# Kernel tuning notes

Measured on AMD Instinct MI355X. Metric: run time of the kernel, lower is better.

The kernel has to match this reference:

```python
import jax, jax.numpy as jnp
import numpy as np

N_SEND = 12288   # 12 * 32^2
N_REC = 49152    # 12 * 64^2
E = 196608       # 4 * N_REC (knn with k=4)
D = 256
EIN, EOUT = 4, 256
LIN_IN, LIN_OUT = 512, 256
B = 2


def setup_inputs() -> dict:
    key = jax.random.key(0)
    ks = jax.random.split(key, 12)
    s = 0.05
    x = jax.random.normal(ks[0], (B, N_SEND, D), jnp.float32)
    edge_attr = jax.random.normal(ks[1], (E, EIN), jnp.float32)
    idx_send = jax.random.randint(ks[2], (E,), 0, N_SEND, dtype=jnp.int32)
    idx_rec = jnp.sort(jax.random.randint(ks[3], (E,), 0, N_REC, dtype=jnp.int32))
    return {
        "x": x,
        "edge_attr": edge_attr,
        "idx_send": idx_send,
        "idx_rec": idx_rec,
        "We1": jax.random.normal(ks[4], (EIN, EOUT), jnp.float32) * s,
        "be1": jnp.zeros((EOUT,), jnp.float32),
        "We2": jax.random.normal(ks[5], (EOUT, EOUT), jnp.float32) * s,
        "be2": jnp.zeros((EOUT,), jnp.float32),
        "Wl1": jax.random.normal(ks[6], (LIN_IN, LIN_OUT), jnp.float32) * s,
        "bl1": jnp.zeros((LIN_OUT,), jnp.float32),
        "Wl2": jax.random.normal(ks[7], (LIN_OUT, LIN_OUT), jnp.float32) * s,
        "bl2": jnp.zeros((LIN_OUT,), jnp.float32),
    }


def reference(x, edge_attr, idx_send, idx_rec, We1, be1, We2, be2, Wl1, bl1, Wl2, bl2):
    # edge embedder MLP: Linear -> GELU -> Linear   [E, EOUT]
    ef = jax.nn.gelu(edge_attr @ We1 + be1) @ We2 + be2
    # gather sender node features by edge           [B, E, D]
    v_s = x[:, idx_send, :]
    # concat gathered features with (batch-broadcast) edge embeddings [B, E, D+EOUT]
    ef_b = jnp.broadcast_to(ef[None], (v_s.shape[0],) + ef.shape)
    v_s_prime = jnp.concatenate([v_s, ef_b], axis=-1)
    # scatter_sum over receiver index along edge dim -> [B, N_REC, LIN_IN]
    agg = jax.vmap(lambda m: jax.ops.segment_sum(m, idx_rec, num_segments=N_REC))(v_s_prime)
    # final FeedForward: Linear -> GELU -> Linear
    return jax.nn.gelu(agg @ Wl1 + bl1) @ Wl2 + bl2
```

## Files before the change

### kernel.cpp

```cpp
#include <hip/hip_runtime.h>
#include <hip/hip_bf16.h>

#define N_SEND 12288
#define N_REC  49152
#define NEDGE  196608

typedef __attribute__((ext_vector_type(8))) short short8;
typedef __attribute__((ext_vector_type(4))) float floatx4;

__device__ inline short f2bs(float f) {
    __hip_bfloat16 h = __float2bfloat16(f);
    return *reinterpret_cast<short*>(&h);
}
__device__ inline float bs2f(unsigned int u16) {
    unsigned int x = u16 << 16;
    return __builtin_bit_cast(float, x);
}
__device__ inline unsigned int pack2(float a, float b) {
    unsigned int lo = (unsigned short)f2bs(a);
    unsigned int hi = (unsigned short)f2bs(b);
    return lo | (hi << 16);
}
__device__ inline float gelu_tanh(float x) {
    const float k0 = 0.7978845608028654f;
    float u = k0 * (x + 0.044715f * x * x * x);
    float e = __expf(2.0f * u);
    float t = 1.0f - 2.0f / (e + 1.0f);
    return 0.5f * x * (1.0f + t);
}

__global__ void prep_kernel(const float* __restrict__ We2, const float* __restrict__ be2,
                            const float* __restrict__ Wl1, const float* __restrict__ Wl2,
                            short* __restrict__ BT1, short* __restrict__ WT2,
                            float* __restrict__ cvec) {
    int i = blockIdx.x;
    int n = threadIdx.x;
    if (i < 256) {
        float acc = 0.f;
        for (int j = 0; j < 256; ++j)
            acc += We2[i * 256 + j] * Wl1[(256 + j) * 256 + n];
        BT1[n * 512 + i]       = f2bs(Wl1[i * 256 + n]);
        BT1[n * 512 + 256 + i] = f2bs(acc);
        WT2[n * 256 + i]       = f2bs(Wl2[i * 256 + n]);
    } else {
        float acc = 0.f;
        for (int j = 0; j < 256; ++j)
            acc += be2[j] * Wl1[(256 + j) * 256 + n];
        cvec[n] = acc;
    }
}

__global__ void xcast_kernel(const float* __restrict__ X, short* __restrict__ Xb) {
    int i = (blockIdx.x * 256 + threadIdx.x) * 8;
    floatx4 v0 = *(const floatx4*)(X + i);
    floatx4 v1 = *(const floatx4*)(X + i + 4);
    short8 p;
#pragma unroll
    for (int j = 0; j < 4; ++j) { p[j] = f2bs(v0[j]); p[j + 4] = f2bs(v1[j]); }
    *(short8*)(Xb + i) = p;
}

__global__ void bounds_kernel(const int* __restrict__ idx_rec, int* __restrict__ bnd) {
    int r = blockIdx.x * 256 + threadIdx.x;
    if (r > N_REC) return;
    int lo = 0, hi = NEDGE;
    while (lo < hi) { int mid = (lo + hi) >> 1; if (idx_rec[mid] < r) lo = mid + 1; else hi = mid; }
    bnd[r] = lo;
}

__global__ __launch_bounds__(256)
void aggregate(const int* __restrict__ idx_send, const int* __restrict__ bnd,
               const float* __restrict__ EA, const float* __restrict__ We1,
               const float* __restrict__ be1, const short* __restrict__ Xb,
               short* __restrict__ Xagg, short* __restrict__ Hagg) {
    __shared__ int sb[33];
    int t = threadIdx.x;
    int r0base = blockIdx.x * 32;
    if (t < 33) sb[t] = bnd[r0base + t];
    __syncthreads();
    int sub = t >> 7;
    int c = t & 127;
    int c2 = 2 * c;
    float w00 = We1[c2],       w01 = We1[c2 + 1];
    float w10 = We1[256 + c2], w11 = We1[256 + c2 + 1];
    float w20 = We1[512 + c2], w21 = We1[512 + c2 + 1];
    float w30 = We1[768 + c2], w31 = We1[768 + c2 + 1];
    float bb0 = be1[c2], bb1 = be1[c2 + 1];
    int rloc0 = sub * 16;

    for (int r = 0; r < 16; ++r) {
        int rr = r0base + rloc0 + r;
        int e0 = sb[rloc0 + r], e1 = sb[rloc0 + r + 1];
        float x00 = 0.f, x01 = 0.f, x10 = 0.f, x11 = 0.f, h0 = 0.f, h1 = 0.f;
#pragma unroll 2
        for (int e = e0; e < e1; ++e) {
            int s = idx_send[e];
            floatx4 a = *(const floatx4*)(EA + e * 4);
            unsigned int xv0 = *(const unsigned int*)(Xb + s * 256 + c2);
            unsigned int xv1 = *(const unsigned int*)(Xb + (N_SEND + s) * 256 + c2);
            x00 += bs2f(xv0 & 0xffffu); x01 += bs2f(xv0 >> 16);
            x10 += bs2f(xv1 & 0xffffu); x11 += bs2f(xv1 >> 16);
            float u0 = a[0] * w00 + a[1] * w10 + a[2] * w20 + a[3] * w30 + bb0;
            float u1 = a[0] * w01 + a[1] * w11 + a[2] * w21 + a[3] * w31 + bb1;
            h0 += gelu_tanh(u0); h1 += gelu_tanh(u1);
        }
        *(unsigned int*)(Xagg + (size_t)rr * 256 + c2)                     = pack2(x00, x01);
        *(unsigned int*)(Xagg + ((size_t)N_REC + rr) * 256 + c2)           = pack2(x10, x11);
        *(unsigned int*)(Hagg + (size_t)rr * 256 + c2)                     = pack2(h0, h1);
    }
}

__device__ inline void mma_tile(const short* Al, const short* Bl,
                                floatx4 acc[16], int wrow, int m, int q) {
#pragma unroll
    for (int kk = 0; kk < 64; kk += 32) {
        short8 a = *(const short8*)(Al + (wrow + m) * 72 + kk + q * 8);
#pragma unroll
        for (int nt = 0; nt < 16; ++nt) {
            short8 b = *(const short8*)(Bl + (nt * 16 + m) * 72 + kk + q * 8);
            acc[nt] = __builtin_amdgcn_mfma_f32_16x16x32_bf16(a, b, acc[nt], 0, 0, 0);
        }
    }
}

__global__ __launch_bounds__(256, 2)
void gemm_fused(const short* __restrict__ Xagg, const short* __restrict__ Hagg,
                const short* __restrict__ BT1, const short* __restrict__ WT2,
                const float* __restrict__ cvec, const float* __restrict__ bl1,
                const float* __restrict__ bl2, const int* __restrict__ bnd,
                float* __restrict__ OUT) {
    __shared__ short Al[64 * 72];
    __shared__ short Bl[256 * 72];
    __shared__ short Tl[64 * 264];
    int t = threadIdx.x;
    int b = blockIdx.x / 768;
    int r0 = (blockIdx.x % 768) * 64;
    int lane = t & 63, w = t >> 6, m = lane & 15, q = lane >> 4;
    floatx4 acc[16];
#pragma unroll
    for (int i = 0; i < 16; ++i) acc[i] = (floatx4){0.f, 0.f, 0.f, 0.f};
    int ar = t >> 2, acs = (t & 3) * 16;
    const short* Arow0 = Xagg + ((size_t)b * N_REC + r0 + ar) * 256 + acs;
    const short* Arow1 = Hagg + ((size_t)(r0 + ar)) * 256 + acs;

    for (int kc = 0; kc < 512; kc += 64) {
        const short* src = (kc < 256) ? (Arow0 + kc) : (Arow1 + (kc - 256));
        *(short8*)(Al + ar * 72 + acs)     = *(const short8*)(src);
        *(short8*)(Al + ar * 72 + acs + 8) = *(const short8*)(src + 8);
#pragma unroll
        for (int cB = 0; cB < 8; ++cB)
            *(short8*)(Bl + t * 72 + cB * 8) = *(const short8*)(BT1 + t * 512 + kc + cB * 8);
        __syncthreads();
        mma_tile(Al, Bl, acc, w * 16, m, q);
        __syncthreads();
    }

    int rbl = w * 16 + q * 4;
    int rbase = r0 + rbl;
    int bv0 = bnd[rbase], bv1 = bnd[rbase + 1], bv2 = bnd[rbase + 2],
        bv3 = bnd[rbase + 3], bv4 = bnd[rbase + 4];
    float cnt[4] = {(float)(bv1 - bv0), (float)(bv2 - bv1),
                    (float)(bv3 - bv2), (float)(bv4 - bv3)};
#pragma unroll
    for (int nt = 0; nt < 16; ++nt) {
        int col = nt * 16 + m;
        float cv = cvec[col], b1v = bl1[col];
#pragma unroll
        for (int r = 0; r < 4; ++r) {
            float v = acc[nt][r] + cnt[r] * cv + b1v;
            Tl[(rbl + r) * 264 + col] = f2bs(gelu_tanh(v));
        }
        acc[nt] = (floatx4){0.f, 0.f, 0.f, 0.f};
    }

    for (int kc = 0; kc < 256; kc += 64) {
#pragma unroll
        for (int cB = 0; cB < 8; ++cB)
            *(short8*)(Bl + t * 72 + cB * 8) = *(const short8*)(WT2 + t * 256 + kc + cB * 8);
        __syncthreads();
#pragma unroll
        for (int kk = 0; kk < 64; kk += 32) {
            short8 a = *(const short8*)(Tl + (w * 16 + m) * 264 + kc + kk + q * 8);
#pragma unroll
            for (int nt = 0; nt < 16; ++nt) {
                short8 bf = *(const short8*)(Bl + (nt * 16 + m) * 72 + kk + q * 8);
                acc[nt] = __builtin_amdgcn_mfma_f32_16x16x32_bf16(a, bf, acc[nt], 0, 0, 0);
            }
        }
        __syncthreads();
    }

#pragma unroll
    for (int nt = 0; nt < 16; ++nt) {
        int col = nt * 16 + m;
        float b2v = bl2[col];
#pragma unroll
        for (int r = 0; r < 4; ++r)
            OUT[((size_t)b * N_REC + rbase + r) * 256 + col] = acc[nt][r] + b2v;
    }
}

extern "C" void kernel_launch(void* const* d_in, const int* in_sizes, int n_in,
                              void* d_out, int out_size, void* d_ws, size_t ws_size,
                              hipStream_t stream) {
    const float* x        = (const float*)d_in[0];
    const float* ea       = (const float*)d_in[1];
    const int*   idx_send = (const int*)d_in[2];
    const int*   idx_rec  = (const int*)d_in[3];
    const float* We1      = (const float*)d_in[4];
    const float* be1      = (const float*)d_in[5];
    const float* We2      = (const float*)d_in[6];
    const float* be2      = (const float*)d_in[7];
    const float* Wl1      = (const float*)d_in[8];
    const float* bl1      = (const float*)d_in[9];
    const float* Wl2      = (const float*)d_in[10];
    const float* bl2      = (const float*)d_in[11];
    float* out = (float*)d_out;
    char*  ws  = (char*)d_ws;

    short* BT1  = (short*)(ws + 0);
    short* WT2  = (short*)(ws + 262144);
    float* cvec = (float*)(ws + 393216);
    int*   bnd  = (int*)  (ws + 397312);
    short* Xb   = (short*)(ws + 1048576);
    short* Xagg = (short*)(ws + 16777216);
    short* Hagg = (short*)(ws + 67108864);

    prep_kernel<<<257, 256, 0, stream>>>(We2, be2, Wl1, Wl2, BT1, WT2, cvec);
    xcast_kernel<<<(2 * N_SEND * 256) / (256 * 8), 256, 0, stream>>>(x, Xb);
    bounds_kernel<<<(N_REC + 1 + 255) / 256, 256, 0, stream>>>(idx_rec, bnd);
    aggregate<<<N_REC / 32, 256, 0, stream>>>(idx_send, bnd, ea, We1, be1, Xb, Xagg, Hagg);
    gemm_fused<<<2 * 768, 256, 0, stream>>>(Xagg, Hagg, BT1, WT2, cvec, bl1, bl2, bnd, out);
}
```

Before: 324.7 us.

## Restage aggregation edges in LDS and split GEMM into two 128-row MFMA32 kernels

The aggregate kernel now stages each block's edge indices and edge attributes in shared memory. Each thread handles 8 receivers and 8 feature columns with 16-byte gathers, covering both batches in one block. The fused two-layer GEMM is split into two kernels that use 128x256 tiles and 32x32x16 MFMA with a k-group LDS layout, which raises reuse per tile. This adds a bf16 intermediate round trip through global memory and an extra kernel launch. In exchange it gets larger tiles and fewer small-MFMA LDS reads.

```diff
diff --git a/kernel.cpp b/kernel.cpp
--- a/kernel.cpp
+++ b/kernel.cpp
@@ -4,22 +4,17 @@
 #define N_SEND 12288
 #define N_REC  49152
 #define NEDGE  196608
-
-typedef __attribute__((ext_vector_type(8))) short short8;
-typedef __attribute__((ext_vector_type(4))) float floatx4;
+#define ECAP   512
+
+typedef __attribute__((ext_vector_type(8)))  short short8;
+typedef __attribute__((ext_vector_type(4)))  short shortx4;
+typedef __attribute__((ext_vector_type(4)))  float floatx4;
+typedef __attribute__((ext_vector_type(16))) float floatx16;
+typedef __attribute__((ext_vector_type(4)))  unsigned int uintx4;
 
 __device__ inline short f2bs(float f) {
     __hip_bfloat16 h = __float2bfloat16(f);
     return *reinterpret_cast<short*>(&h);
-}
-__device__ inline float bs2f(unsigned int u16) {
-    unsigned int x = u16 << 16;
-    return __builtin_bit_cast(float, x);
-}
-__device__ inline unsigned int pack2(float a, float b) {
-    unsigned int lo = (unsigned short)f2bs(a);
-    unsigned int hi = (unsigned short)f2bs(b);
-    return lo | (hi << 16);
 }
 __device__ inline float gelu_tanh(float x) {
     const float k0 = 0.7978845608028654f;
@@ -74,129 +69,237 @@
                const float* __restrict__ be1, const short* __restrict__ Xb,
                short* __restrict__ Xagg, short* __restrict__ Hagg) {
     __shared__ int sb[33];
+    __shared__ int s_idx[ECAP];
+    __shared__ float s_ea[ECAP * 4];
     int t = threadIdx.x;
-    int r0base = blockIdx.x * 32;
-    if (t < 33) sb[t] = bnd[r0base + t];
+    int r0 = blockIdx.x * 32;
+    if (t < 33) sb[t] = bnd[r0 + t];
     __syncthreads();
-    int sub = t >> 7;
-    int c = t & 127;
-    int c2 = 2 * c;
-    float w00 = We1[c2],       w01 = We1[c2 + 1];
-    float w10 = We1[256 + c2], w11 = We1[256 + c2 + 1];
-    float w20 = We1[512 + c2], w21 = We1[512 + c2 + 1];
-    float w30 = We1[768 + c2], w31 = We1[768 + c2 + 1];
-    float bb0 = be1[c2], bb1 = be1[c2 + 1];
-    int rloc0 = sub * 16;
-
-    for (int r = 0; r < 16; ++r) {
-        int rr = r0base + rloc0 + r;
-        int e0 = sb[rloc0 + r], e1 = sb[rloc0 + r + 1];
-        float x00 = 0.f, x01 = 0.f, x10 = 0.f, x11 = 0.f, h0 = 0.f, h1 = 0.f;
-#pragma unroll 2
-        for (int e = e0; e < e1; ++e) {
-            int s = idx_send[e];
-            floatx4 a = *(const floatx4*)(EA + e * 4);
-            unsigned int xv0 = *(const unsigned int*)(Xb + s * 256 + c2);
-            unsigned int xv1 = *(const unsigned int*)(Xb + (N_SEND + s) * 256 + c2);
-            x00 += bs2f(xv0 & 0xffffu); x01 += bs2f(xv0 >> 16);
-            x10 += bs2f(xv1 & 0xffffu); x11 += bs2f(xv1 >> 16);
-            float u0 = a[0] * w00 + a[1] * w10 + a[2] * w20 + a[3] * w30 + bb0;
-            float u1 = a[0] * w01 + a[1] * w11 + a[2] * w21 + a[3] * w31 + bb1;
-            h0 += gelu_tanh(u0); h1 += gelu_tanh(u1);
-        }
-        *(unsigned int*)(Xagg + (size_t)rr * 256 + c2)                     = pack2(x00, x01);
-        *(unsigned int*)(Xagg + ((size_t)N_REC + rr) * 256 + c2)           = pack2(x10, x11);
-        *(unsigned int*)(Hagg + (size_t)rr * 256 + c2)                     = pack2(h0, h1);
-    }
-}
-
-__device__ inline void mma_tile(const short* Al, const short* Bl,
-                                floatx4 acc[16], int wrow, int m, int q) {
-#pragma unroll
-    for (int kk = 0; kk < 64; kk += 32) {
-        short8 a = *(const short8*)(Al + (wrow + m) * 72 + kk + q * 8);
-#pragma unroll
-        for (int nt = 0; nt < 16; ++nt) {
-            short8 b = *(const short8*)(Bl + (nt * 16 + m) * 72 + kk + q * 8);
-            acc[nt] = __builtin_amdgcn_mfma_f32_16x16x32_bf16(a, b, acc[nt], 0, 0, 0);
-        }
-    }
-}
+    int e0 = sb[0], eN = sb[32];
+
+    int cg = t & 31;
+    int b  = (t >> 5) & 1;
+    int rq = t >> 6;
+    int c8 = cg * 8;
+    int hc = c8 + 4 * b;
+
+    floatx4 w0 = *(const floatx4*)(We1 + hc);
+    floatx4 w1 = *(const floatx4*)(We1 + 256 + hc);
+    floatx4 w2 = *(const floatx4*)(We1 + 512 + hc);
+    floatx4 w3 = *(const floatx4*)(We1 + 768 + hc);
+    floatx4 bb = *(const floatx4*)(be1 + hc);
+
+    const short* xb_t = Xb + (size_t)b * N_SEND * 256 + c8;
+
+    float xacc[8][8];
+    float hacc[8][4];
+#pragma unroll
+    for (int r = 0; r < 8; ++r) {
+#pragma unroll
+        for (int c = 0; c < 8; ++c) xacc[r][c] = 0.f;
+#pragma unroll
+        for (int c = 0; c < 4; ++c) hacc[r][c] = 0.f;
+    }
+
+    for (int base = e0; base < eN; base += ECAP) {
+        int cnt = min(ECAP, eN - base);
+        __syncthreads();
+        for (int i = t; i < cnt; i += 256) {
+            s_idx[i] = idx_send[base + i];
+            *(floatx4*)(s_ea + 4 * i) = *(const floatx4*)(EA + (size_t)(base + i) * 4);
+        }
+        __syncthreads();
+#pragma unroll
+        for (int r = 0; r < 8; ++r) {
+            int rr = rq * 8 + r;
+            int es = max(sb[rr], base);
+            int ee = min(sb[rr + 1], base + cnt);
+            for (int e = es; e < ee; ++e) {
+                int li = e - base;
+                int s = s_idx[li];
+                uintx4 xv = *(const uintx4*)(xb_t + (size_t)s * 256);
+                floatx4 a = *(const floatx4*)(s_ea + 4 * li);
+#pragma unroll
+                for (int dw = 0; dw < 4; ++dw) {
+                    xacc[r][2 * dw]     += __builtin_bit_cast(float, xv[dw] << 16);
+                    xacc[r][2 * dw + 1] += __builtin_bit_cast(float, xv[dw] & 0xffff0000u);
+                }
+#pragma unroll
+                for (int j = 0; j < 4; ++j) {
+                    float u = a[0] * w0[j] + a[1] * w1[j] + a[2] * w2[j] + a[3] * w3[j] + bb[j];
+                    hacc[r][j] += gelu_tanh(u);
+                }
+            }
+        }
+    }
+#pragma unroll
+    for (int r = 0; r < 8; ++r) {
+        int rr = r0 + rq * 8 + r;
+        short8 xp;
+#pragma unroll
+        for (int c = 0; c < 8; ++c) xp[c] = f2bs(xacc[r][c]);
+        *(short8*)(Xagg + ((size_t)b * N_REC + rr) * 256 + c8) = xp;
+        shortx4 hp;
+#pragma unroll
+        for (int c = 0; c < 4; ++c) hp[c] = f2bs(hacc[r][c]);
+        *(shortx4*)(Hagg + (size_t)rr * 256 + hc) = hp;
+    }
+}
+
 
 __global__ __launch_bounds__(256, 2)
-void gemm_fused(const short* __restrict__ Xagg, const short* __restrict__ Hagg,
-                const short* __restrict__ BT1, const short* __restrict__ WT2,
-                const float* __restrict__ cvec, const float* __restrict__ bl1,
-                const float* __restrict__ bl2, const int* __restrict__ bnd,
-                float* __restrict__ OUT) {
-    __shared__ short Al[64 * 72];
-    __shared__ short Bl[256 * 72];
-    __shared__ short Tl[64 * 264];
+void gemm_t(const short* __restrict__ Xagg, const short* __restrict__ Hagg,
+            const short* __restrict__ BT1, const float* __restrict__ cvec,
+            const float* __restrict__ bl1, const int* __restrict__ bnd,
+            short* __restrict__ Tg) {
+    __shared__ short Al[8 * 128 * 8];
+    __shared__ short Bl[8 * 256 * 8];
     int t = threadIdx.x;
-    int b = blockIdx.x / 768;
-    int r0 = (blockIdx.x % 768) * 64;
-    int lane = t & 63, w = t >> 6, m = lane & 15, q = lane >> 4;
-    floatx4 acc[16];
-#pragma unroll
-    for (int i = 0; i < 16; ++i) acc[i] = (floatx4){0.f, 0.f, 0.f, 0.f};
-    int ar = t >> 2, acs = (t & 3) * 16;
-    const short* Arow0 = Xagg + ((size_t)b * N_REC + r0 + ar) * 256 + acs;
-    const short* Arow1 = Hagg + ((size_t)(r0 + ar)) * 256 + acs;
+    int lane = t & 63, w = t >> 6;
+    int m = lane & 31, q = lane >> 5;
+    int R0 = blockIdx.x * 128;
+    int rh0 = (R0 < N_REC) ? R0 : R0 - N_REC;
+    floatx16 acc[8];
+#pragma unroll
+    for (int i = 0; i < 8; ++i)
+#pragma unroll
+        for (int j = 0; j < 16; ++j) acc[i][j] = 0.f;
+
+    int sr = t >> 1;
+    int skh = (t & 1) * 4;
+    int wr = (w & 1) * 64;
+    int wc = (w >> 1) * 128;
 
     for (int kc = 0; kc < 512; kc += 64) {
-        const short* src = (kc < 256) ? (Arow0 + kc) : (Arow1 + (kc - 256));
-        *(short8*)(Al + ar * 72 + acs)     = *(const short8*)(src);
-        *(short8*)(Al + ar * 72 + acs + 8) = *(const short8*)(src + 8);
-#pragma unroll
-        for (int cB = 0; cB < 8; ++cB)
-            *(short8*)(Bl + t * 72 + cB * 8) = *(const short8*)(BT1 + t * 512 + kc + cB * 8);
-        __syncthreads();
-        mma_tile(Al, Bl, acc, w * 16, m, q);
-        __syncthreads();
-    }
-
-    int rbl = w * 16 + q * 4;
-    int rbase = r0 + rbl;
-    int bv0 = bnd[rbase], bv1 = bnd[rbase + 1], bv2 = bnd[rbase + 2],
-        bv3 = bnd[rbase + 3], bv4 = bnd[rbase + 4];
-    float cnt[4] = {(float)(bv1 - bv0), (float)(bv2 - bv1),
-                    (float)(bv3 - bv2), (float)(bv4 - bv3)};
-#pragma unroll
-    for (int nt = 0; nt < 16; ++nt) {
-        int col = nt * 16 + m;
-        float cv = cvec[col], b1v = bl1[col];
-#pragma unroll
-        for (int r = 0; r < 4; ++r) {
-            float v = acc[nt][r] + cnt[r] * cv + b1v;
-            Tl[(rbl + r) * 264 + col] = f2bs(gelu_tanh(v));
-        }
-        acc[nt] = (floatx4){0.f, 0.f, 0.f, 0.f};
-    }
+        const short* Asrc = (kc < 256)
+            ? (Xagg + (size_t)R0 * 256 + kc)
+            : (Hagg + (size_t)rh0 * 256 + (kc - 256));
+#pragma unroll
+        for (int i = 0; i < 4; ++i) {
+            short8 v = *(const short8*)(Asrc + sr * 256 + (skh + i) * 8);
+            *(short8*)(Al + ((skh + i) * 128 + sr) * 8) = v;
+        }
+#pragma unroll
+        for (int i = 0; i < 8; ++i) {
+            short8 v = *(const short8*)(BT1 + (size_t)t * 512 + kc + i * 8);
+            *(short8*)(Bl + (i * 256 + t) * 8) = v;
+        }
+        __syncthreads();
+#pragma unroll
+        for (int kk = 0; kk < 4; ++kk) {
+            int kg = 2 * kk + q;
+            short8 a0 = *(const short8*)(Al + (kg * 128 + wr + m) * 8);
+            short8 a1 = *(const short8*)(Al + (kg * 128 + wr + 32 + m) * 8);
+            short8 b0 = *(const short8*)(Bl + (kg * 256 + wc + m) * 8);
+            short8 b1 = *(const short8*)(Bl + (kg * 256 + wc + 32 + m) * 8);
+            short8 b2 = *(const short8*)(Bl + (kg * 256 + wc + 64 + m) * 8);
+            short8 b3 = *(const short8*)(Bl + (kg * 256 + wc + 96 + m) * 8);
+            acc[0] = __builtin_amdgcn_mfma_f32_32x32x16_bf16(b0, a0, acc[0], 0, 0, 0);
+            acc[1] = __builtin_amdgcn_mfma_f32_32x32x16_bf16(b1, a0, acc[1], 0, 0, 0);
+            acc[2] = __builtin_amdgcn_mfma_f32_32x32x16_bf16(b2, a0, acc[2], 0, 0, 0);
+            acc[3] = __builtin_amdgcn_mfma_f32_32x32x16_bf16(b3, a0, acc[3], 0, 0, 0);
+            acc[4] = __builtin_amdgcn_mfma_f32_32x32x16_bf16(b0, a1, acc[4], 0, 0, 0);
+            acc[5] = __builtin_amdgcn_mfma_f32_32x32x16_bf16(b1, a1, acc[5], 0, 0, 0);
+            acc[6] = __builtin_amdgcn_mfma_f32_32x32x16_bf16(b2, a1, acc[6], 0, 0, 0);
+            acc[7] = __builtin_amdgcn_mfma_f32_32x32x16_bf16(b3, a1, acc[7], 0, 0, 0);
+        }
+        __syncthreads();
+    }
+
+#pragma unroll
+    for (int rt = 0; rt < 2; ++rt) {
+        int row = R0 + wr + rt * 32 + m;
+        int rmod = (row >= N_REC) ? row - N_REC : row;
+        float cnt = (float)(bnd[rmod + 1] - bnd[rmod]);
+#pragma unroll
+        for (int ct = 0; ct < 4; ++ct) {
+#pragma unroll
+            for (int qd = 0; qd < 4; ++qd) {
+                int c0 = wc + ct * 32 + qd * 8 + q * 4;
+                floatx4 cv  = *(const floatx4*)(cvec + c0);
+                floatx4 b1v = *(const floatx4*)(bl1 + c0);
+                shortx4 pk;
+#pragma unroll
+                for (int j = 0; j < 4; ++j) {
+                    float v = acc[rt * 4 + ct][qd * 4 + j] + cnt * cv[j] + b1v[j];
+                    pk[j] = f2bs(gelu_tanh(v));
+                }
+                *(shortx4*)(Tg + (size_t)row * 256 + c0) = pk;
+            }
+        }
+    }
+}
+
+__global__ __launch_bounds__(256, 2)
+void gemm_o(const short* __restrict__ Tg, const short* __restrict__ WT2,
+            const float* __restrict__ bl2, float* __restrict__ OUT) {
+    __shared__ short Al[8 * 128 * 8];
+    __shared__ short Bl[8 * 256 * 8];
+    int t = threadIdx.x;
+    int lane = t & 63, w = t >> 6;
+    int m = lane & 31, q = lane >> 5;
+    int R0 = blockIdx.x * 128;
+    floatx16 acc[8];
+#pragma unroll
+    for (int i = 0; i < 8; ++i)
+#pragma unroll
+        for (int j = 0; j < 16; ++j) acc[i][j] = 0.f;
+
+    int sr = t >> 1;
+    int skh = (t & 1) * 4;
+    int wr = (w & 1) * 64;
+    int wc = (w >> 1) * 128;
 
     for (int kc = 0; kc < 256; kc += 64) {
-#pragma unroll
-        for (int cB = 0; cB < 8; ++cB)
-            *(short8*)(Bl + t * 72 + cB * 8) = *(const short8*)(WT2 + t * 256 + kc + cB * 8);
-        __syncthreads();
-#pragma unroll
-        for (int kk = 0; kk < 64; kk += 32) {
-            short8 a = *(const short8*)(Tl + (w * 16 + m) * 264 + kc + kk + q * 8);
-#pragma unroll
-            for (int nt = 0; nt < 16; ++nt) {
-                short8 bf = *(const short8*)(Bl + (nt * 16 + m) * 72 + kk + q * 8);
-                acc[nt] = __builtin_amdgcn_mfma_f32_16x16x32_bf16(a, bf, acc[nt], 0, 0, 0);
+        const short* Asrc = Tg + (size_t)R0 * 256 + kc;
+#pragma unroll
+        for (int i = 0; i < 4; ++i) {
+            short8 v = *(const short8*)(Asrc + sr * 256 + (skh + i) * 8);
+            *(short8*)(Al + ((skh + i) * 128 + sr) * 8) = v;
+        }
+#pragma unroll
+        for (int i = 0; i < 8; ++i) {
+            short8 v = *(const short8*)(WT2 + (size_t)t * 256 + kc + i * 8);
+            *(short8*)(Bl + (i * 256 + t) * 8) = v;
+        }
+        __syncthreads();
+#pragma unroll
+        for (int kk = 0; kk < 4; ++kk) {
+            int kg = 2 * kk + q;
+            short8 a0 = *(const short8*)(Al + (kg * 128 + wr + m) * 8);
+            short8 a1 = *(const short8*)(Al + (kg * 128 + wr + 32 + m) * 8);
+            short8 b0 = *(const short8*)(Bl + (kg * 256 + wc + m) * 8);
+            short8 b1 = *(const short8*)(Bl + (kg * 256 + wc + 32 + m) * 8);
+            short8 b2 = *(const short8*)(Bl + (kg * 256 + wc + 64 + m) * 8);
+            short8 b3 = *(const short8*)(Bl + (kg * 256 + wc + 96 + m) * 8);
+            acc[0] = __builtin_amdgcn_mfma_f32_32x32x16_bf16(b0, a0, acc[0], 0, 0, 0);
+            acc[1] = __builtin_amdgcn_mfma_f32_32x32x16_bf16(b1, a0, acc[1], 0, 0, 0);
+            acc[2] = __builtin_amdgcn_mfma_f32_32x32x16_bf16(b2, a0, acc[2], 0, 0, 0);
+            acc[3] = __builtin_amdgcn_mfma_f32_32x32x16_bf16(b3, a0, acc[3], 0, 0, 0);
+            acc[4] = __builtin_amdgcn_mfma_f32_32x32x16_bf16(b0, a1, acc[4], 0, 0, 0);
+            acc[5] = __builtin_amdgcn_mfma_f32_32x32x16_bf16(b1, a1, acc[5], 0, 0, 0);
+            acc[6] = __builtin_amdgcn_mfma_f32_32x32x16_bf16(b2, a1, acc[6], 0, 0, 0);
+            acc[7] = __builtin_amdgcn_mfma_f32_32x32x16_bf16(b3, a1, acc[7], 0, 0, 0);
+        }
+        __syncthreads();
+    }
+
+#pragma unroll
+    for (int rt = 0; rt < 2; ++rt) {
+        int row = R0 + wr + rt * 32 + m;
+#pragma unroll
+        for (int ct = 0; ct < 4; ++ct) {
+#pragma unroll
+            for (int qd = 0; qd < 4; ++qd) {
+                int c0 = wc + ct * 32 + qd * 8 + q * 4;
+                floatx4 bv = *(const floatx4*)(bl2 + c0);
+                floatx4 o;
+#pragma unroll
+                for (int j = 0; j < 4; ++j)
+                    o[j] = acc[rt * 4 + ct][qd * 4 + j] + bv[j];
+                *(floatx4*)(OUT + (size_t)row * 256 + c0) = o;
             }
         }
-        __syncthreads();
-    }
-
-#pragma unroll
-    for (int nt = 0; nt < 16; ++nt) {
-        int col = nt * 16 + m;
-        float b2v = bl2[col];
-#pragma unroll
-        for (int r = 0; r < 4; ++r)
-            OUT[((size_t)b * N_REC + rbase + r) * 256 + col] = acc[nt][r] + b2v;
     }
 }
 
@@ -225,10 +328,12 @@
     short* Xb   = (short*)(ws + 1048576);
     short* Xagg = (short*)(ws + 16777216);
     short* Hagg = (short*)(ws + 67108864);
+    short* Tg   = (short*)(ws + 92274688);
 
     prep_kernel<<<257, 256, 0, stream>>>(We2, be2, Wl1, Wl2, BT1, WT2, cvec);
     xcast_kernel<<<(2 * N_SEND * 256) / (256 * 8), 256, 0, stream>>>(x, Xb);
     bounds_kernel<<<(N_REC + 1 + 255) / 256, 256, 0, stream>>>(idx_rec, bnd);
     aggregate<<<N_REC / 32, 256, 0, stream>>>(idx_send, bnd, ea, We1, be1, Xb, Xagg, Hagg);
-    gemm_fused<<<2 * 768, 256, 0, stream>>>(Xagg, Hagg, BT1, WT2, cvec, bl1, bl2, bnd, out);
-}
+    gemm_t<<<(2 * N_REC) / 128, 256, 0, stream>>>(Xagg, Hagg, BT1, cvec, bl1, bnd, Tg);
+    gemm_o<<<(2 * N_REC) / 128, 256, 0, stream>>>(Tg, WT2, bl2, out);
+}
```

Measured after the change: 340.3 us. 4.8% more time.
